# Optimization experiments

Hardware: AMD Instinct MI355X
Metric: run time of the kernel (lower is better)

## Reference

```python
import jax, jax.numpy as jnp
import numpy as np


def _diffuse(x, A):
    # x: [B,C,N,L], A: [B,V,W] -> out[b,c,v,l] = sum_w x[b,c,w,l] * A[b,v,w]
    return jnp.einsum('ncwl,nvw->ncvl', x, A)


def setup_inputs() -> dict:
    key = jax.random.key(0)
    kx, k0, k1, k2, kw = jax.random.split(key, 5)
    B, C, N, L = 32, 40, 512, 12
    C_OUT = 20
    C_CAT = 7 * C  # (order*support_len + 1) * c_in = (2*3+1)*40
    x = jax.random.normal(kx, (B, C, N, L), dtype=jnp.float32)
    def mk_support(k):
        a = jax.random.uniform(k, (B, N, N), dtype=jnp.float32)
        return a / jnp.sum(a, axis=-1, keepdims=True)  # row-normalized transition
    A0, A1, A2 = mk_support(k0), mk_support(k1), mk_support(k2)
    # Conv2d(c_cat, c_out, kernel=(1,2), dilation=2) weights, stored [c_out, c_cat, 2]
    W = jax.random.normal(kw, (C_OUT, C_CAT, 2), dtype=jnp.float32) * 0.05
    b = jnp.zeros((C_OUT,), dtype=jnp.float32)
    return {'x': x, 'A0': A0, 'A1': A1, 'A2': A2, 'W': W, 'b': b}


def reference(x, A0, A1, A2, W, b):
    # dgcn.forward (eval mode, dropout is identity): order=2, support_len=3
    out = [x]
    for A in (A0, A1, A2):
        x1 = _diffuse(x, A)
        out.append(x1)
        x2 = _diffuse(x1, A)
        out.append(x2)
    h = jnp.concatenate(out, axis=1)  # [B, 7C, N, L]
    # linear_: Conv2d kernel (1,2), dilation 2, no padding -> taps at t and t+2, L_out = L-2
    y = (jnp.einsum('ncvl,oc->novl', h[..., :-2], W[:, :, 0])
         + jnp.einsum('ncvl,oc->novl', h[..., 2:], W[:, :, 1])
         + b[None, :, None, None])
    return y
```

## Files before the change

### kernel.cpp

```cpp
#include <hip/hip_runtime.h>
#include <hip/hip_bf16.h>


typedef unsigned short u16;
typedef u16 u16x4 __attribute__((ext_vector_type(4)));
typedef u16 u16x8 __attribute__((ext_vector_type(8)));
typedef __bf16 bf16x8 __attribute__((ext_vector_type(8)));
typedef float f32x4 __attribute__((ext_vector_type(4)));

#define GLD_LDS16(g, l)  __builtin_amdgcn_global_load_lds( \
    (const __attribute__((address_space(1))) void*)(g),    \
    (__attribute__((address_space(3))) void*)(l), 16, 0, 0)

__device__ __forceinline__ u16 f2bf(float f) {
    unsigned int u = __float_as_uint(f);
    u += 0x7fffu + ((u >> 16) & 1u);
    return (u16)(u >> 16);
}
__device__ __forceinline__ float bf2f(u16 h) {
    return __uint_as_float(((unsigned int)h) << 16);
}

__global__ __launch_bounds__(256) void proj_x(
    const float* __restrict__ x, const float* __restrict__ W,
    u16* __restrict__ P1, u16* __restrict__ P2, float* __restrict__ proj0)
{
    __shared__ u16 sA[144 * 104];
    __shared__ u16 sB[64 * 104];
    const int t = threadIdx.x;
    const int v0 = blockIdx.x * 64, l = blockIdx.y, b = blockIdx.z;

    for (int id = t; id < 144 * 13; id += 256) {
        int m = id / 13, kc = id % 13, k0 = kc * 8;
        u16x8 val = {};
        if (m < 140 && k0 < 80) {
            int o = m % 20, sg = m / 20;
            const float* wp = W + o * 560 + sg * 80 + k0;
            float4 w0 = *(const float4*)wp;
            float4 w1 = *(const float4*)(wp + 4);
            val[0] = f2bf(w0.x); val[1] = f2bf(w0.y); val[2] = f2bf(w0.z); val[3] = f2bf(w0.w);
            val[4] = f2bf(w1.x); val[5] = f2bf(w1.y); val[6] = f2bf(w1.z); val[7] = f2bf(w1.w);
        }
        *(u16x8*)(&sA[m * 104 + k0]) = val;
    }
    for (int id = t; id < 5120; id += 256) {
        int v = id & 63, k = id >> 6;
        int c = k >> 1, tap = k & 1;
        float xv = x[((size_t)(b * 40 + c) * 512 + v0 + v) * 12 + l + 2 * tap];
        sB[v * 104 + k] = f2bf(xv);
    }
    for (int id = t; id < 64 * 3; id += 256) {
        int v = id / 3, j = id % 3;
        u16x8 z = {};
        *(u16x8*)(&sB[v * 104 + 80 + j * 8]) = z;
    }
    __syncthreads();

    const int lane = t & 63, wid = t >> 6;
    const int lrow = lane & 15, lk = (lane >> 4) * 8;
    f32x4 acc[9] = {};
    #pragma unroll
    for (int ks = 0; ks < 3; ++ks) {
        bf16x8 xf = *(const bf16x8*)(&sB[(wid * 16 + lrow) * 104 + ks * 32 + lk]);
        #pragma unroll
        for (int mf = 0; mf < 9; ++mf) {
            bf16x8 af = *(const bf16x8*)(&sA[(mf * 16 + lrow) * 104 + ks * 32 + lk]);
            acc[mf] = __builtin_amdgcn_mfma_f32_16x16x32_bf16(af, xf, acc[mf], 0, 0, 0);
        }
    }

    const int v = v0 + wid * 16 + lrow;
    const int r4 = (lane >> 4) * 4;
    #pragma unroll
    for (int mf = 0; mf < 9; ++mf)
        #pragma unroll
        for (int i = 0; i < 4; ++i) {
            int m = mf * 16 + r4 + i;
            if (m < 140) {
                int o = m % 20, sg = m / 20;
                float val = acc[mf][i];
                if (sg == 0) {
                    proj0[((size_t)(b * 20 + o) * 10 + l) * 512 + v] = val;
                } else {
                    int s = (sg - 1) >> 1;
                    u16* dst = ((sg - 1) & 1) ? P2 : P1;
                    dst[((size_t)(s * 32 + b) * 200 + o * 10 + l) * 512 + v] = f2bf(val);
                }
            }
        }
}

template <int EPI>
__device__ __forceinline__ void gemm_body(
    const float* __restrict__ A0, const float* __restrict__ A1, const float* __restrict__ A2,
    const u16* __restrict__ Xsrc, u16* __restrict__ Tdst, float* __restrict__ Ydst)
{
    __shared__ float sAf[2][128 * 32];
    __shared__ u16   sXs[2][112 * 32];

    const int bid = blockIdx.x;
    const int eid = (bid & 7) * 96 + (bid >> 3);
    const int z = eid >> 3, rem = eid & 7;
    const int vblk = (rem >> 1) * 128;
    const int colbase = (rem & 1) * 112;
    const int s = z >> 5, b = z & 31;

    const float* Af = (s == 0 ? A0 : (s == 1 ? A1 : A2)) + (size_t)b * 512 * 512;
    const u16* Xb = Xsrc + (size_t)z * 200 * 512;

    const int t = threadIdx.x;
    const int lane = t & 63, wid = t >> 6;
    const int lr = lane & 15;
    const int kc0 = (lane >> 4) * 2;

    auto stage = [&](int kt, int buf) {
        const int w0 = kt * 32;
        float* ab = &sAf[buf][0];
        u16*   xb = &sXs[buf][0];
        #pragma unroll
        for (int i = 0; i < 4; ++i) {
            int op  = wid * 4 + i;
            int row = op * 8 + (lane >> 3);
            int pc  = lane & 7;
            const float* src = Af + (size_t)(vblk + row) * 512 + w0 + ((pc ^ (row & 7)) << 2);
            GLD_LDS16(src, ab + op * 256);
        }
        #pragma unroll
        for (int i = 0; i < 2; ++i) {
            int op = wid + i * 4;
            if (op < 7) {
                int row = op * 16 + (lane >> 2);
                int ch  = lane & 3;
                const u16* src = Xb + (size_t)(colbase + row) * 512 + w0 + ch * 8;
                GLD_LDS16(src, xb + op * 512);
            }
        }
    };

    f32x4 acc[7][2] = {};

    stage(0, 0);
    __syncthreads();

    for (int kt = 0; kt < 16; ++kt) {
        const int cur = kt & 1;
        if (kt < 15) stage(kt + 1, cur ^ 1);

        bf16x8 af[2];
        #pragma unroll
        for (int mf = 0; mf < 2; ++mf) {
            int r = wid * 32 + mf * 16 + lr;
            const float* rb = &sAf[cur][r * 32];
            f32x4 a0 = *(const f32x4*)(rb + ((kc0 ^ (r & 7)) << 2));
            f32x4 a1 = *(const f32x4*)(rb + (((kc0 + 1) ^ (r & 7)) << 2));
            union { u16x8 u; bf16x8 bv; } cv;
            cv.u = (u16x8){ f2bf(a0[0]), f2bf(a0[1]), f2bf(a0[2]), f2bf(a0[3]),
                            f2bf(a1[0]), f2bf(a1[1]), f2bf(a1[2]), f2bf(a1[3]) };
            af[mf] = cv.bv;
        }
        #pragma unroll
        for (int cf = 0; cf < 7; ++cf) {
            bf16x8 xf = *(const bf16x8*)(&sXs[cur][(cf * 16 + lr) * 32 + (lane >> 4) * 8]);
            #pragma unroll
            for (int mf = 0; mf < 2; ++mf)
                acc[cf][mf] = __builtin_amdgcn_mfma_f32_16x16x32_bf16(
                    xf, af[mf], acc[cf][mf], 0, 0, 0);
        }
        __syncthreads();
    }

    const int r4 = (lane >> 4) * 4;
    if (EPI == 0) {
        u16* Tz = Tdst + (size_t)z * 200 * 512;
        #pragma unroll
        for (int cf = 0; cf < 7; ++cf)
            #pragma unroll
            for (int mf = 0; mf < 2; ++mf)
                #pragma unroll
                for (int i = 0; i < 4; ++i) {
                    int col = colbase + cf * 16 + r4 + i;
                    if (col < 200) {
                        size_t idx = (size_t)col * 512 + vblk + wid * 32 + mf * 16 + lr;
                        Tz[idx] = f2bf(acc[cf][mf][i] + bf2f(Tz[idx]));
                    }
                }
    } else {
        float* Yz = Ydst + (size_t)z * 200 * 512;
        #pragma unroll
        for (int cf = 0; cf < 7; ++cf)
            #pragma unroll
            for (int mf = 0; mf < 2; ++mf)
                #pragma unroll
                for (int i = 0; i < 4; ++i) {
                    int col = colbase + cf * 16 + r4 + i;
                    if (col < 200)
                        Yz[(size_t)col * 512 + vblk + wid * 32 + mf * 16 + lr] = acc[cf][mf][i];
                }
    }
}

__global__ __launch_bounds__(256) void gemm_t(
    const float* __restrict__ A0, const float* __restrict__ A1, const float* __restrict__ A2,
    const u16* __restrict__ P2, u16* __restrict__ T)
{
    gemm_body<0>(A0, A1, A2, P2, T, nullptr);
}

__global__ __launch_bounds__(256) void gemm_yp(
    const float* __restrict__ A0, const float* __restrict__ A1, const float* __restrict__ A2,
    const u16* __restrict__ T, float* __restrict__ Ypart)
{
    gemm_body<1>(A0, A1, A2, T, nullptr, Ypart);
}

__global__ __launch_bounds__(256) void reduce_y(
    const float* __restrict__ Ypart, const float* __restrict__ proj0,
    const float* __restrict__ bias, float* __restrict__ y)
{
    int i = blockIdx.x * 256 + threadIdx.x;
    if (i >= 32 * 20 * 512) return;
    int v = i & 511;
    int r = i >> 9;
    int o = r % 20, b = r / 20;
    float bb = bias[o];
    float* yp = y + ((size_t)r * 512 + v) * 10;
    #pragma unroll
    for (int l = 0; l < 10; ++l) {
        float sum = proj0[((size_t)r * 10 + l) * 512 + v] + bb;
        #pragma unroll
        for (int s = 0; s < 3; ++s)
            sum += Ypart[((size_t)(s * 32 + b) * 200 + o * 10 + l) * 512 + v];
        yp[l] = sum;
    }
}

extern "C" void kernel_launch(void* const* d_in, const int* in_sizes, int n_in,
                              void* d_out, int out_size, void* d_ws, size_t ws_size,
                              hipStream_t stream) {
    const float* x    = (const float*)d_in[0];
    const float* A0   = (const float*)d_in[1];
    const float* A1   = (const float*)d_in[2];
    const float* A2   = (const float*)d_in[3];
    const float* W    = (const float*)d_in[4];
    const float* bias = (const float*)d_in[5];
    float* y = (float*)d_out;

    const size_t PSZ = (size_t)96 * 200 * 512;
    u16* P1 = (u16*)d_ws;
    u16* P2 = P1 + PSZ;
    float* proj0 = (float*)(P2 + PSZ);
    float* Ypart = proj0 + (size_t)32 * 20 * 10 * 512;

    proj_x<<<dim3(8, 10, 32), 256, 0, stream>>>(x, W, P1, P2, proj0);
    gemm_t<<<dim3(768), 256, 0, stream>>>(A0, A1, A2, P2, P1);
    gemm_yp<<<dim3(768), 256, 0, stream>>>(A0, A1, A2, P1, Ypart);
    reduce_y<<<dim3(1280), 256, 0, stream>>>(Ypart, proj0, bias, y);
}
```

Before: 107.5 us.

## Pre-transpose x to bf16 layout and pipeline projection over time steps

Adds an xpose kernel that converts x to bf16 in a [B,L,N,Cpad48] layout. proj_x is reworked to use one block per (v-tile, batch) that loops over all 10 output time steps. It keeps weight fragments in registers and double-buffers x tiles in LDS through global_load_lds. This replaces the strided scalar fp32 gathers of x and the weight reloads repeated in every block, at the cost of an extra kernel launch, 10x fewer blocks (256) and heavy register pressure. xq reuses the Ypart workspace, which is later overwritten.

```diff
diff --git a/kernel.cpp b/kernel.cpp
--- a/kernel.cpp
+++ b/kernel.cpp
@@ -21,73 +21,150 @@
     return __uint_as_float(((unsigned int)h) << 16);
 }
 
+__global__ __launch_bounds__(256) void xpose(const float* __restrict__ x,
+                                             u16* __restrict__ xq)
+{
+    const int t = threadIdx.x, vloc = t & 63, cg = t >> 6;
+    const int v = blockIdx.x * 64 + vloc, b = blockIdx.y;
+
+    u16 vals[12][12];
+    #pragma unroll
+    for (int ci = 0; ci < 12; ++ci) {
+        int c = cg * 12 + ci;
+        if (c < 40) {
+            const float* xp = x + ((size_t)(b * 40 + c) * 512 + v) * 12;
+            float4 f0 = *(const float4*)xp;
+            float4 f1 = *(const float4*)(xp + 4);
+            float4 f2 = *(const float4*)(xp + 8);
+            vals[0][ci] = f2bf(f0.x);  vals[1][ci] = f2bf(f0.y);
+            vals[2][ci] = f2bf(f0.z);  vals[3][ci] = f2bf(f0.w);
+            vals[4][ci] = f2bf(f1.x);  vals[5][ci] = f2bf(f1.y);
+            vals[6][ci] = f2bf(f1.z);  vals[7][ci] = f2bf(f1.w);
+            vals[8][ci] = f2bf(f2.x);  vals[9][ci] = f2bf(f2.y);
+            vals[10][ci] = f2bf(f2.z); vals[11][ci] = f2bf(f2.w);
+        } else {
+            #pragma unroll
+            for (int l = 0; l < 12; ++l) vals[l][ci] = 0;
+        }
+    }
+    #pragma unroll
+    for (int l = 0; l < 12; ++l) {
+        u16* dst = xq + ((size_t)(b * 12 + l) * 512 + v) * 48 + cg * 12;
+        u16x4 a = { vals[l][0], vals[l][1], vals[l][2], vals[l][3] };
+        u16x4 c4 = { vals[l][4], vals[l][5], vals[l][6], vals[l][7] };
+        u16x4 d = { vals[l][8], vals[l][9], vals[l][10], vals[l][11] };
+        *(u16x4*)(dst) = a;
+        *(u16x4*)(dst + 4) = c4;
+        *(u16x4*)(dst + 8) = d;
+    }
+}
+
 __global__ __launch_bounds__(256) void proj_x(
-    const float* __restrict__ x, const float* __restrict__ W,
+    const u16* __restrict__ xq, const float* __restrict__ W,
     u16* __restrict__ P1, u16* __restrict__ P2, float* __restrict__ proj0)
 {
     __shared__ u16 sA[144 * 104];
-    __shared__ u16 sB[64 * 104];
-    const int t = threadIdx.x;
-    const int v0 = blockIdx.x * 64, l = blockIdx.y, b = blockIdx.z;
-
-    for (int id = t; id < 144 * 13; id += 256) {
-        int m = id / 13, kc = id % 13, k0 = kc * 8;
-        u16x8 val = {};
-        if (m < 140 && k0 < 80) {
+    __shared__ u16 sB[2][2 * 64 * 48];
+
+    const int t = threadIdx.x, lane = t & 63, wid = t >> 6;
+    const int b = blockIdx.y, v0 = blockIdx.x * 64;
+
+    for (int id = t; id < 144 * 5; id += 256) {
+        int m = id / 5, c0 = (id % 5) * 8;
+        u16x8 e = {}, o8 = {};
+        if (m < 140) {
             int o = m % 20, sg = m / 20;
-            const float* wp = W + o * 560 + sg * 80 + k0;
-            float4 w0 = *(const float4*)wp;
-            float4 w1 = *(const float4*)(wp + 4);
-            val[0] = f2bf(w0.x); val[1] = f2bf(w0.y); val[2] = f2bf(w0.z); val[3] = f2bf(w0.w);
-            val[4] = f2bf(w1.x); val[5] = f2bf(w1.y); val[6] = f2bf(w1.z); val[7] = f2bf(w1.w);
-        }
-        *(u16x8*)(&sA[m * 104 + k0]) = val;
-    }
-    for (int id = t; id < 5120; id += 256) {
-        int v = id & 63, k = id >> 6;
-        int c = k >> 1, tap = k & 1;
-        float xv = x[((size_t)(b * 40 + c) * 512 + v0 + v) * 12 + l + 2 * tap];
-        sB[v * 104 + k] = f2bf(xv);
-    }
-    for (int id = t; id < 64 * 3; id += 256) {
-        int v = id / 3, j = id % 3;
+            const float* wp = W + o * 560 + sg * 80 + c0 * 2;
+            float4 a = *(const float4*)wp;
+            float4 bb = *(const float4*)(wp + 4);
+            float4 c = *(const float4*)(wp + 8);
+            float4 d = *(const float4*)(wp + 12);
+            e[0] = f2bf(a.x);  o8[0] = f2bf(a.y);  e[1] = f2bf(a.z);  o8[1] = f2bf(a.w);
+            e[2] = f2bf(bb.x); o8[2] = f2bf(bb.y); e[3] = f2bf(bb.z); o8[3] = f2bf(bb.w);
+            e[4] = f2bf(c.x);  o8[4] = f2bf(c.y);  e[5] = f2bf(c.z);  o8[5] = f2bf(c.w);
+            e[6] = f2bf(d.x);  o8[6] = f2bf(d.y);  e[7] = f2bf(d.z);  o8[7] = f2bf(d.w);
+        }
+        *(u16x8*)(&sA[m * 104 + c0]) = e;
+        *(u16x8*)(&sA[m * 104 + 40 + c0]) = o8;
+    }
+    for (int id = t; id < 144 * 3; id += 256) {
+        int m = id / 3, k0 = 80 + (id % 3) * 8;
         u16x8 z = {};
-        *(u16x8*)(&sB[v * 104 + 80 + j * 8]) = z;
-    }
+        *(u16x8*)(&sA[m * 104 + k0]) = z;
+    }
+
+    auto stage = [&](int l, int buf) {
+        u16* dst = &sB[buf][0];
+        #pragma unroll
+        for (int i = 0; i < 3; ++i) {
+            int op = wid * 3 + i;
+            int tap = op / 6, rem = op % 6;
+            const u16* src = xq + ((size_t)(b * 12 + l + 2 * tap) * 512 + v0) * 48
+                             + rem * 512 + lane * 8;
+            GLD_LDS16(src, dst + tap * 3072 + rem * 512);
+        }
+    };
+
+    stage(0, 0);
     __syncthreads();
 
-    const int lane = t & 63, wid = t >> 6;
-    const int lrow = lane & 15, lk = (lane >> 4) * 8;
-    f32x4 acc[9] = {};
-    #pragma unroll
-    for (int ks = 0; ks < 3; ++ks) {
-        bf16x8 xf = *(const bf16x8*)(&sB[(wid * 16 + lrow) * 104 + ks * 32 + lk]);
-        #pragma unroll
-        for (int mf = 0; mf < 9; ++mf) {
-            bf16x8 af = *(const bf16x8*)(&sA[(mf * 16 + lrow) * 104 + ks * 32 + lk]);
-            acc[mf] = __builtin_amdgcn_mfma_f32_16x16x32_bf16(af, xf, acc[mf], 0, 0, 0);
-        }
-    }
-
-    const int v = v0 + wid * 16 + lrow;
-    const int r4 = (lane >> 4) * 4;
+    const int lr = lane & 15, q = lane >> 4;
+    bf16x8 af[9][3];
     #pragma unroll
     for (int mf = 0; mf < 9; ++mf)
         #pragma unroll
-        for (int i = 0; i < 4; ++i) {
-            int m = mf * 16 + r4 + i;
-            if (m < 140) {
-                int o = m % 20, sg = m / 20;
-                float val = acc[mf][i];
-                if (sg == 0) {
-                    proj0[((size_t)(b * 20 + o) * 10 + l) * 512 + v] = val;
-                } else {
-                    int s = (sg - 1) >> 1;
-                    u16* dst = ((sg - 1) & 1) ? P2 : P1;
-                    dst[((size_t)(s * 32 + b) * 200 + o * 10 + l) * 512 + v] = f2bf(val);
+        for (int s = 0; s < 3; ++s)
+            af[mf][s] = *(const bf16x8*)(&sA[(mf * 16 + lr) * 104 + s * 32 + q * 8]);
+
+    const int voff = (wid * 16 + lr) * 48;
+    int boff[3];
+    #pragma unroll
+    for (int s = 0; s < 3; ++s) {
+        int k = s * 32 + q * 8;
+        int tap, c;
+        if (k < 40)      { tap = 0; c = k; }
+        else if (k < 80) { tap = 1; c = k - 40; }
+        else             { tap = 1; c = 40; }
+        boff[s] = tap * 3072 + voff + c;
+    }
+
+    const int v = v0 + wid * 16 + lr;
+    for (int l = 0; l < 10; ++l) {
+        const int cur = l & 1;
+        if (l < 9) stage(l + 1, cur ^ 1);
+
+        const u16* bb = &sB[cur][0];
+        bf16x8 xf[3];
+        #pragma unroll
+        for (int s = 0; s < 3; ++s) xf[s] = *(const bf16x8*)(bb + boff[s]);
+
+        f32x4 acc[9] = {};
+        #pragma unroll
+        for (int s = 0; s < 3; ++s)
+            #pragma unroll
+            for (int mf = 0; mf < 9; ++mf)
+                acc[mf] = __builtin_amdgcn_mfma_f32_16x16x32_bf16(
+                    af[mf][s], xf[s], acc[mf], 0, 0, 0);
+
+        #pragma unroll
+        for (int mf = 0; mf < 9; ++mf)
+            #pragma unroll
+            for (int i = 0; i < 4; ++i) {
+                int m = mf * 16 + q * 4 + i;
+                if (m < 140) {
+                    int o = m % 20, sg = m / 20;
+                    float val = acc[mf][i];
+                    if (sg == 0) {
+                        proj0[((size_t)(b * 20 + o) * 10 + l) * 512 + v] = val;
+                    } else {
+                        int s2 = (sg - 1) >> 1;
+                        u16* dst = ((sg - 1) & 1) ? P2 : P1;
+                        dst[((size_t)(s2 * 32 + b) * 200 + o * 10 + l) * 512 + v] = f2bf(val);
+                    }
                 }
             }
-        }
+        __syncthreads();
+    }
 }
 
 template <int EPI>
@@ -250,8 +327,10 @@
     u16* P2 = P1 + PSZ;
     float* proj0 = (float*)(P2 + PSZ);
     float* Ypart = proj0 + (size_t)32 * 20 * 10 * 512;
-
-    proj_x<<<dim3(8, 10, 32), 256, 0, stream>>>(x, W, P1, P2, proj0);
+    u16* xq = (u16*)Ypart;
+
+    xpose<<<dim3(8, 32), 256, 0, stream>>>(x, xq);
+    proj_x<<<dim3(8, 32), 256, 0, stream>>>(xq, W, P1, P2, proj0);
     gemm_t<<<dim3(768), 256, 0, stream>>>(A0, A1, A2, P2, P1);
     gemm_yp<<<dim3(768), 256, 0, stream>>>(A0, A1, A2, P1, Ypart);
     reduce_y<<<dim3(1280), 256, 0, stream>>>(Ypart, proj0, bias, y);
```

Result: faster. 105.2 us (-2.2%).
